# Kernel optimization log

Hardware: AMD Instinct MI355X
Metric: run time of the kernel (lower is better)

The kernel has to match this reference:

```python
import jax, jax.numpy as jnp
import numpy as np
from jax import lax

H = 8          # num_heads
STATE = 16     # SSM state_dim
EPS = 1e-5


def layer_norm(x, g, b):
    mu = jnp.mean(x, axis=-1, keepdims=True)
    var = jnp.mean((x - mu) ** 2, axis=-1, keepdims=True)
    return (x - mu) / jnp.sqrt(var + EPS) * g + b


def linear(x, w, b):
    # torch nn.Linear convention: w [out,in]
    return x @ w.T + b


def cross_attn(q_in, kv_in, qw, qb, kw, kb, vw, vb, ow, ob, g, beta):
    B, Lq, D = q_in.shape
    Lk = kv_in.shape[1]
    hd = D // H
    Q = linear(q_in, qw, qb).reshape(B, Lq, H, hd).transpose(0, 2, 1, 3)
    K = linear(kv_in, kw, kb).reshape(B, Lk, H, hd).transpose(0, 2, 1, 3)
    V = linear(kv_in, vw, vb).reshape(B, Lk, H, hd).transpose(0, 2, 1, 3)
    scores = jnp.einsum('bhqd,bhkd->bhqk', Q, K) / (hd ** 0.5)
    w = jax.nn.softmax(scores, axis=-1)
    out = jnp.einsum('bhqk,bhkd->bhqd', w, V)
    out = out.transpose(0, 2, 1, 3).reshape(B, Lq, D)
    out = linear(out, ow, ob)
    out = layer_norm(out + q_in, g, beta)
    return out, w


def ssm(x, in_w, in_b, A, Bm, C, gw, gb, ow, ob):
    B, L, D = x.shape
    xp = linear(x, in_w, in_b)                      # [B,L,2D]
    x_in = xp[..., D:]                              # second chunk
    gate = jax.nn.sigmoid(linear(x, gw, gb))
    x_in = x_in * gate
    def step(h, xt):
        h = h @ A.T + xt @ Bm.T                     # [B,STATE]
        return h, h @ C.T                           # y [B,D]
    h0 = jnp.zeros((B, STATE), dtype=x.dtype)
    _, ys = lax.scan(step, h0, x_in.transpose(1, 0, 2))
    ys = ys.transpose(1, 0, 2)
    return linear(ys, ow, ob)


def mamba_block(x, p, i):
    y = ssm(layer_norm(x, p['m_ln1_g'][i], p['m_ln1_b'][i]),
            p['m_in_w'][i], p['m_in_b'][i], p['m_A'][i], p['m_B'][i], p['m_C'][i],
            p['m_gate_w'][i], p['m_gate_b'][i], p['m_sout_w'][i], p['m_sout_b'][i])
    x = x + y
    h = layer_norm(x, p['m_ln2_g'][i], p['m_ln2_b'][i])
    h = linear(h, p['m_f1_w'][i], p['m_f1_b'][i])
    h = jax.nn.gelu(h, approximate=False)
    h = linear(h, p['m_f2_w'][i], p['m_f2_b'][i])
    return x + h


def setup_inputs() -> dict:
    key = jax.random.key(0)
    ks = iter(jax.random.split(key, 64))
    B, L, D, BD, VD = 1024, 32, 256, 128, 256
    nB = 6
    def rn(shape, s=0.02):
        return jax.random.normal(next(ks), shape, dtype=jnp.float32) * s
    inp = {
        'ble_features': jax.random.normal(next(ks), (B, L, BD), dtype=jnp.float32),
        'visual_features': jax.random.normal(next(ks), (B, L, VD), dtype=jnp.float32),
        # modality projections
        'bp_w': rn((D, BD)), 'bp_b': jnp.zeros(D), 'bp_emb': rn((D,)),
        'bp_g': jnp.ones(D), 'bp_beta': jnp.zeros(D),
        'vp_w': rn((D, VD)), 'vp_b': jnp.zeros(D), 'vp_emb': rn((D,)),
        'vp_g': jnp.ones(D), 'vp_beta': jnp.zeros(D),
        # two cross-attentions stacked on axis 0: [0]=ble->vis, [1]=vis->ble
        'a_qw': rn((2, D, D)), 'a_qb': jnp.zeros((2, D)),
        'a_kw': rn((2, D, D)), 'a_kb': jnp.zeros((2, D)),
        'a_vw': rn((2, D, D)), 'a_vb': jnp.zeros((2, D)),
        'a_ow': rn((2, D, D)), 'a_ob': jnp.zeros((2, D)),
        'a_g': jnp.ones((2, D)), 'a_beta': jnp.zeros((2, D)),
        # 6 mamba blocks stacked on axis 0
        'm_ln1_g': jnp.ones((nB, D)), 'm_ln1_b': jnp.zeros((nB, D)),
        'm_in_w': rn((nB, 2 * D, D)), 'm_in_b': jnp.zeros((nB, 2 * D)),
        'm_A': rn((nB, STATE, STATE)), 'm_B': rn((nB, STATE, D)), 'm_C': rn((nB, D, STATE)),
        'm_gate_w': rn((nB, D, D)), 'm_gate_b': jnp.zeros((nB, D)),
        'm_sout_w': rn((nB, D, D)), 'm_sout_b': jnp.zeros((nB, D)),
        'm_ln2_g': jnp.ones((nB, D)), 'm_ln2_b': jnp.zeros((nB, D)),
        'm_f1_w': rn((nB, 4 * D, D)), 'm_f1_b': jnp.zeros((nB, 4 * D)),
        'm_f2_w': rn((nB, D, 4 * D)), 'm_f2_b': jnp.zeros((nB, D)),
        # final projection
        'fin_g': jnp.ones(D), 'fin_beta': jnp.zeros(D),
        'fin_w': rn((D, D)), 'fin_b': jnp.zeros(D),
    }
    return inp


def reference(ble_features, visual_features,
              bp_w, bp_b, bp_emb, bp_g, bp_beta,
              vp_w, vp_b, vp_emb, vp_g, vp_beta,
              a_qw, a_qb, a_kw, a_kb, a_vw, a_vb, a_ow, a_ob, a_g, a_beta,
              m_ln1_g, m_ln1_b, m_in_w, m_in_b, m_A, m_B, m_C,
              m_gate_w, m_gate_b, m_sout_w, m_sout_b,
              m_ln2_g, m_ln2_b, m_f1_w, m_f1_b, m_f2_w, m_f2_b,
              fin_g, fin_beta, fin_w, fin_b):
    ble = layer_norm(linear(ble_features, bp_w, bp_b) + bp_emb, bp_g, bp_beta)
    vis = layer_norm(linear(visual_features, vp_w, vp_b) + vp_emb, vp_g, vp_beta)
    # seq_len == target_length -> align_sequences is identity
    ble_att, w_b2v = cross_attn(ble, vis, a_qw[0], a_qb[0], a_kw[0], a_kb[0],
                                a_vw[0], a_vb[0], a_ow[0], a_ob[0], a_g[0], a_beta[0])
    vis_att, w_v2b = cross_attn(vis, ble, a_qw[1], a_qb[1], a_kw[1], a_kb[1],
                                a_vw[1], a_vb[1], a_ow[1], a_ob[1], a_g[1], a_beta[1])
    fused = ble_att + vis_att
    p = dict(m_ln1_g=m_ln1_g, m_ln1_b=m_ln1_b, m_in_w=m_in_w, m_in_b=m_in_b,
             m_A=m_A, m_B=m_B, m_C=m_C, m_gate_w=m_gate_w, m_gate_b=m_gate_b,
             m_sout_w=m_sout_w, m_sout_b=m_sout_b, m_ln2_g=m_ln2_g, m_ln2_b=m_ln2_b,
             m_f1_w=m_f1_w, m_f1_b=m_f1_b, m_f2_w=m_f2_w, m_f2_b=m_f2_b)
    for i in range(m_A.shape[0]):
        fused = mamba_block(fused, p, i)
    g = jnp.mean(fused, axis=1)
    g = layer_norm(g, fin_g, fin_beta)
    g = jax.nn.gelu(linear(g, fin_w, fin_b), approximate=False)
    wb = jnp.mean(w_b2v, axis=(1, 2, 3))
    wv = jnp.mean(w_v2b, axis=(1, 2, 3))
    tot = wb + wv + 1e-6
    return (g, wb / tot, wv / tot)
```

## Files before the change

### kernel.cpp

```cpp
#include <hip/hip_runtime.h>
#include <hip/hip_bf16.h>
#include <math.h>

static constexpr int Bsz  = 1024;
static constexpr int Lseq = 32;
static constexpr int Dm   = 256;
static constexpr int NROW = Bsz * Lseq;

typedef __attribute__((ext_vector_type(8))) short bf16x8;
typedef __attribute__((ext_vector_type(4))) float f32x4;

__device__ __forceinline__ float sigm_f(float x) {
    return 1.0f / (1.0f + __expf(-x));
}
__device__ __forceinline__ float gelu_f(float x) {
    const float u = x * (0.7978845608028654f + 0.0356774081f * x * x);
    return x * sigm_f(2.0f * u);
}
__device__ __forceinline__ float b2f(ushort u) {
    union { float f; uint v; } t; t.v = ((uint)u) << 16; return t.f;
}
__device__ __forceinline__ ushort f2b(float f) {
    union { float f; uint v; } t; t.f = f;
    const uint lsb = (t.v >> 16) & 1u;
    t.v += 0x7fffu + lsb;
    return (ushort)(t.v >> 16);
}

#define GLDS(gp, lp) __builtin_amdgcn_global_load_lds( \
    (const __attribute__((address_space(1))) void*)(gp), \
    (__attribute__((address_space(3))) void*)(lp), 16, 0, 0)

template<int ACT, bool OUTBF, int OMAP, int DUAL>
__global__ __launch_bounds__(256)
void mgemm(const ushort* __restrict__ X, const ushort* __restrict__ W,
           const ushort* __restrict__ W2,
           const float* __restrict__ b1, const float* __restrict__ b2,
           float* __restrict__ Cf, ushort* __restrict__ Cb,
           ushort* __restrict__ Cb2, int K, int M)
{
    __shared__ ushort As[128 * 32];
    __shared__ ushort Bs[128 * 32];
    __shared__ ushort Bs2[DUAL ? 128 * 32 : 8];
    const int tid = threadIdx.x;
    const int w = tid >> 6, l = tid & 63;
    const int n0 = blockIdx.y << 7;
    const int m0 = blockIdx.x << 7;

    const int ric  = l >> 2;
    const int slot = l & 3;
    const int rL0 = (w << 4) + ric;
    const int rL1 = rL0 + 64;
    const int sw0 = slot ^ ((rL0 >> 1) & 3);
    const int sw1 = slot ^ ((rL1 >> 1) & 3);
    const ushort* gA0 = X + (size_t)(n0 + rL0) * K + (sw0 << 3);
    const ushort* gA1 = X + (size_t)(n0 + rL1) * K + (sw1 << 3);
    const ushort* gB0 = W + (size_t)(m0 + rL0) * K + (sw0 << 3);
    const ushort* gB1 = W + (size_t)(m0 + rL1) * K + (sw1 << 3);
    const ushort* gC0 = nullptr; const ushort* gC1 = nullptr;
    if constexpr (DUAL) {
        gC0 = W2 + (size_t)(m0 + rL0) * K + (sw0 << 3);
        gC1 = W2 + (size_t)(m0 + rL1) * K + (sw1 << 3);
    }
    ushort* lA0 = As + ((size_t)w << 9);
    ushort* lA1 = As + ((size_t)(w + 4) << 9);
    ushort* lB0 = Bs + ((size_t)w << 9);
    ushort* lB1 = Bs + ((size_t)(w + 4) << 9);
    ushort* lC0 = Bs2 + ((size_t)w << 9);
    ushort* lC1 = Bs2 + ((size_t)(w + 4) << 9);

    const int wr = (w >> 1) & 1, wc = w & 1;
    const int cl = l & 15, kg = l >> 4;
    int aoff[4], boff[4];
    #pragma unroll
    for (int m = 0; m < 4; ++m) {
        const int r = wr * 64 + m * 16 + cl;
        aoff[m] = r * 32 + ((kg ^ ((r >> 1) & 3)) << 3);
    }
    #pragma unroll
    for (int n = 0; n < 4; ++n) {
        const int r = wc * 64 + n * 16 + cl;
        boff[n] = r * 32 + ((kg ^ ((r >> 1) & 3)) << 3);
    }

    f32x4 acc[4][4];
    f32x4 acc2[DUAL ? 4 : 1][DUAL ? 4 : 1];
    #pragma unroll
    for (int m = 0; m < 4; ++m)
        #pragma unroll
        for (int n = 0; n < 4; ++n) {
            acc[m][n] = (f32x4){0.f, 0.f, 0.f, 0.f};
            if constexpr (DUAL) acc2[m][n] = (f32x4){0.f, 0.f, 0.f, 0.f};
        }

    for (int kc = 0; kc < K; kc += 32) {
        GLDS(gA0, lA0); GLDS(gA1, lA1);
        GLDS(gB0, lB0); GLDS(gB1, lB1);
        gA0 += 32; gA1 += 32; gB0 += 32; gB1 += 32;
        if constexpr (DUAL) {
            GLDS(gC0, lC0); GLDS(gC1, lC1);
            gC0 += 32; gC1 += 32;
        }
        __syncthreads();
        bf16x8 av[4], bv[4];
        #pragma unroll
        for (int m = 0; m < 4; ++m) av[m] = *(const bf16x8*)(As + aoff[m]);
        #pragma unroll
        for (int n = 0; n < 4; ++n) bv[n] = *(const bf16x8*)(Bs + boff[n]);
        #pragma unroll
        for (int m = 0; m < 4; ++m)
            #pragma unroll
            for (int n = 0; n < 4; ++n)
                acc[m][n] = __builtin_amdgcn_mfma_f32_16x16x32_bf16(
                    av[m], bv[n], acc[m][n], 0, 0, 0);
        if constexpr (DUAL) {
            bf16x8 cv[4];
            #pragma unroll
            for (int n = 0; n < 4; ++n) cv[n] = *(const bf16x8*)(Bs2 + boff[n]);
            #pragma unroll
            for (int m = 0; m < 4; ++m)
                #pragma unroll
                for (int n = 0; n < 4; ++n)
                    acc2[m][n] = __builtin_amdgcn_mfma_f32_16x16x32_bf16(
                        av[m], cv[n], acc2[m][n], 0, 0, 0);
        }
        __syncthreads();
    }

    const int colb = m0 + wc * 64 + cl;
    const int rowb = n0 + wr * 64 + (kg << 2);
    float biasA[4], biasB[4];
    #pragma unroll
    for (int n = 0; n < 4; ++n) {
        biasA[n] = (b1 != nullptr) ? b1[colb + n * 16] : 0.0f;
        if constexpr (DUAL) biasB[n] = b2[colb + n * 16];
    }
    #pragma unroll
    for (int m = 0; m < 4; ++m) {
        #pragma unroll
        for (int j = 0; j < 4; ++j) {
            const size_t row = (size_t)(rowb + m * 16 + j);
            #pragma unroll
            for (int n = 0; n < 4; ++n) {
                const int col = colb + n * 16;
                size_t idx;
                if (OMAP == 1) idx = row * 1024 + ((size_t)(col >> 4) << 5) + (col & 15);
                else           idx = row * (size_t)M + col;
                const float vA = acc[m][n][j] + biasA[n];
                if constexpr (DUAL == 1) {
                    const float vB = acc2[m][n][j] + biasB[n];
                    Cb[idx] = f2b(sigm_f(vA) * vB);
                } else if constexpr (DUAL == 2) {
                    Cb[idx]  = f2b(vA);
                    Cb2[idx] = f2b(acc2[m][n][j] + biasB[n]);
                } else {
                    float v = vA;
                    if (ACT == 1) v = sigm_f(v);
                    else if (ACT == 2) v = gelu_f(v);
                    if (OUTBF) Cb[idx] = f2b(v);
                    else       Cf[idx] = v;
                }
            }
        }
    }
}

template<bool ADD_E, bool ACC_F, bool WRV, int LNOUT, bool HASB2>
__global__ __launch_bounds__(256)
void growln_k(const ushort* __restrict__ X, const ushort* __restrict__ W,
              const float* __restrict__ b1, const float* __restrict__ b2,
              const float* __restrict__ E, const float* __restrict__ g,
              const float* __restrict__ bt, float* __restrict__ Fres,
              ushort* __restrict__ Yb, int K)
{
    __shared__ ushort As[64 * 32];
    __shared__ ushort Bs[256 * 32];
    const int tid = threadIdx.x;
    const int w = tid >> 6, l = tid & 63;
    const int n0 = blockIdx.x << 6;

    const int ric = l >> 2, slot = l & 3;
    const int rA  = (w << 4) + ric;
    const int swA = slot ^ ((rA >> 1) & 3);
    const ushort* gA = X + (size_t)(n0 + rA) * K + (swA << 3);
    ushort* lA = As + (w << 9);
    const int rB0 = (w << 4) + ric;
    const int rB1 = rB0 + 64, rB2 = rB0 + 128, rB3 = rB0 + 192;
    const ushort* gB0 = W + (size_t)rB0 * K + ((slot ^ ((rB0 >> 1) & 3)) << 3);
    const ushort* gB1 = W + (size_t)rB1 * K + ((slot ^ ((rB1 >> 1) & 3)) << 3);
    const ushort* gB2 = W + (size_t)rB2 * K + ((slot ^ ((rB2 >> 1) & 3)) << 3);
    const ushort* gB3 = W + (size_t)rB3 * K + ((slot ^ ((rB3 >> 1) & 3)) << 3);
    ushort* lB0 = Bs + (w << 9);
    ushort* lB1 = Bs + ((4 + w) << 9);
    ushort* lB2 = Bs + ((8 + w) << 9);
    ushort* lB3 = Bs + ((12 + w) << 9);

    const int cl = l & 15, kg = l >> 4;
    const int ar = (w << 4) + cl;
    const int aoff = ar * 32 + ((kg ^ ((ar >> 1) & 3)) << 3);
    int boff[16];
    #pragma unroll
    for (int n = 0; n < 16; ++n) {
        const int br = n * 16 + cl;
        boff[n] = br * 32 + ((kg ^ ((br >> 1) & 3)) << 3);
    }

    f32x4 acc[16];
    #pragma unroll
    for (int n = 0; n < 16; ++n) acc[n] = (f32x4){0.f, 0.f, 0.f, 0.f};

    for (int kc = 0; kc < K; kc += 32) {
        GLDS(gA, lA);   gA  += 32;
        GLDS(gB0, lB0); gB0 += 32;
        GLDS(gB1, lB1); gB1 += 32;
        GLDS(gB2, lB2); gB2 += 32;
        GLDS(gB3, lB3); gB3 += 32;
        __syncthreads();
        const bf16x8 av = *(const bf16x8*)(As + aoff);
        #pragma unroll
        for (int n = 0; n < 16; ++n) {
            const bf16x8 bv = *(const bf16x8*)(Bs + boff[n]);
            acc[n] = __builtin_amdgcn_mfma_f32_16x16x32_bf16(av, bv, acc[n], 0, 0, 0);
        }
        __syncthreads();
    }

    float bA[16];
    #pragma unroll
    for (int n = 0; n < 16; ++n) {
        float v = (b1 != nullptr) ? b1[n * 16 + cl] : 0.0f;
        if (HASB2) v += b2[n * 16 + cl];
        bA[n] = v;
    }
    float gg[16], bb[16];
    if (LNOUT > 0) {
        #pragma unroll
        for (int n = 0; n < 16; ++n) { gg[n] = g[n * 16 + cl]; bb[n] = bt[n * 16 + cl]; }
    }

    #pragma unroll
    for (int j = 0; j < 4; ++j) {
        const int r = n0 + (w << 4) + (kg << 2) + j;
        const size_t rb = (size_t)r << 8;
        float v[16];
        float s = 0.0f;
        #pragma unroll
        for (int n = 0; n < 16; ++n) {
            float x = acc[n][j] + bA[n];
            if (ADD_E) x += E[rb + n * 16 + cl];
            if (ACC_F) x += Fres[rb + n * 16 + cl];
            v[n] = x; s += x;
        }
        if (WRV) {
            #pragma unroll
            for (int n = 0; n < 16; ++n) Fres[rb + n * 16 + cl] = v[n];
        }
        if (LNOUT > 0) {
            #pragma unroll
            for (int o = 1; o < 16; o <<= 1) s += __shfl_xor(s, o);
            const float mu = s * (1.0f / 256.0f);
            float q = 0.0f;
            #pragma unroll
            for (int n = 0; n < 16; ++n) { const float d = v[n] - mu; q += d * d; }
            #pragma unroll
            for (int o = 1; o < 16; o <<= 1) q += __shfl_xor(q, o);
            const float rstd = rsqrtf(q * (1.0f / 256.0f) + 1e-5f);
            #pragma unroll
            for (int n = 0; n < 16; ++n) {
                const float y = (v[n] - mu) * rstd * gg[n] + bb[n];
                const size_t idx = rb + n * 16 + cl;
                if (LNOUT & 1) Yb[idx] = f2b(y);
                if (LNOUT == 2 || LNOUT == 3) Fres[idx] = y;
                if (LNOUT == 4) Fres[idx] += y;
            }
        }
    }
}

__global__ __launch_bounds__(256)
void ln_k(const float* __restrict__ X, const float* __restrict__ g,
          const float* __restrict__ bt, ushort* __restrict__ Yb)
{
    const int lane = threadIdx.x & 63;
    const int row  = (blockIdx.x << 2) + (threadIdx.x >> 6);
    const size_t base = (size_t)row * Dm + (lane << 2);
    float4 v = *reinterpret_cast<const float4*>(&X[base]);
    float s = v.x + v.y + v.z + v.w;
    #pragma unroll
    for (int o = 1; o < 64; o <<= 1) s += __shfl_xor(s, o);
    const float mu = s * (1.0f / 256.0f);
    const float d0 = v.x - mu, d1 = v.y - mu, d2 = v.z - mu, d3 = v.w - mu;
    float q = d0*d0 + d1*d1 + d2*d2 + d3*d3;
    #pragma unroll
    for (int o = 1; o < 64; o <<= 1) q += __shfl_xor(q, o);
    const float rstd = rsqrtf(q * (1.0f / 256.0f) + 1e-5f);
    const int c = lane << 2;
    const float4 gg = *reinterpret_cast<const float4*>(&g[c]);
    const float4 bb = *reinterpret_cast<const float4*>(&bt[c]);
    ushort4 ub;
    ub.x = f2b(d0*rstd*gg.x + bb.x); ub.y = f2b(d1*rstd*gg.y + bb.y);
    ub.z = f2b(d2*rstd*gg.z + bb.z); ub.w = f2b(d3*rstd*gg.w + bb.w);
    *reinterpret_cast<ushort4*>(&Yb[base]) = ub;
}

__global__ __launch_bounds__(256)
void attn_k(const ushort* __restrict__ Q, const ushort* __restrict__ K,
            const ushort* __restrict__ V, ushort* __restrict__ O)
{
    __shared__ float Qs[32][33], Ks[32][33], Vs[32][33], Ss[32][33];
    const int bh = blockIdx.x;
    const int b = bh >> 3, h = bh & 7;
    const int tid = threadIdx.x;
    const int r  = tid >> 3;
    const int c4 = (tid & 7) << 2;
    const size_t base = ((size_t)b * Lseq + r) * Dm + h * 32 + c4;
    {
        const ushort4 q = *reinterpret_cast<const ushort4*>(&Q[base]);
        Qs[r][c4+0]=b2f(q.x); Qs[r][c4+1]=b2f(q.y); Qs[r][c4+2]=b2f(q.z); Qs[r][c4+3]=b2f(q.w);
        const ushort4 k = *reinterpret_cast<const ushort4*>(&K[base]);
        Ks[r][c4+0]=b2f(k.x); Ks[r][c4+1]=b2f(k.y); Ks[r][c4+2]=b2f(k.z); Ks[r][c4+3]=b2f(k.w);
        const ushort4 v = *reinterpret_cast<const ushort4*>(&V[base]);
        Vs[r][c4+0]=b2f(v.x); Vs[r][c4+1]=b2f(v.y); Vs[r][c4+2]=b2f(v.z); Vs[r][c4+3]=b2f(v.w);
    }
    __syncthreads();
    float sc[4] = {0.f, 0.f, 0.f, 0.f};
    #pragma unroll
    for (int d = 0; d < 32; ++d) {
        const float qv = Qs[r][d];
        #pragma unroll
        for (int j = 0; j < 4; ++j) sc[j] = fmaf(qv, Ks[c4+j][d], sc[j]);
    }
    #pragma unroll
    for (int j = 0; j < 4; ++j) sc[j] *= 0.17677669529663687f;
    float mx = fmaxf(fmaxf(sc[0], sc[1]), fmaxf(sc[2], sc[3]));
    #pragma unroll
    for (int o = 1; o < 8; o <<= 1) mx = fmaxf(mx, __shfl_xor(mx, o));
    float sum = 0.f;
    #pragma unroll
    for (int j = 0; j < 4; ++j) { sc[j] = __expf(sc[j] - mx); sum += sc[j]; }
    #pragma unroll
    for (int o = 1; o < 8; o <<= 1) sum += __shfl_xor(sum, o);
    const float inv = 1.0f / sum;
    #pragma unroll
    for (int j = 0; j < 4; ++j) Ss[r][c4+j] = sc[j] * inv;
    __syncthreads();
    float o4[4] = {0.f, 0.f, 0.f, 0.f};
    #pragma unroll
    for (int k = 0; k < 32; ++k) {
        const float wv = Ss[r][k];
        #pragma unroll
        for (int j = 0; j < 4; ++j) o4[j] = fmaf(wv, Vs[k][c4+j], o4[j]);
    }
    ushort4 ob; ob.x=f2b(o4[0]); ob.y=f2b(o4[1]); ob.z=f2b(o4[2]); ob.w=f2b(o4[3]);
    *reinterpret_cast<ushort4*>(&O[base]) = ob;
}

__global__ __launch_bounds__(256)
void xb_gemm(const ushort* __restrict__ X, const ushort* __restrict__ Bw,
             ushort* __restrict__ XB)
{
    __shared__ ushort As[128 * 32];
    __shared__ ushort Bsf[16 * 256];
    const int tid = threadIdx.x;
    const int w = tid >> 6, l = tid & 63;
    const int n0 = blockIdx.x << 7;
    #pragma unroll
    for (int rep = 0; rep < 2; ++rep) {
        const int u = (rep << 8) + tid;
        const int r = u >> 5;
        const int c8 = (u & 31) << 3;
        const int di = (r * 256 + c8) ^ ((r & 7) << 3);
        *(bf16x8*)(Bsf + di) = *(const bf16x8*)(Bw + r * 256 + c8);
    }
    const int ric = l >> 2, slot = l & 3;
    const int rL0 = (w << 4) + ric, rL1 = rL0 + 64;
    const int sw0 = slot ^ ((rL0 >> 1) & 3), sw1 = slot ^ ((rL1 >> 1) & 3);
    const ushort* gA0 = X + (size_t)(n0 + rL0) * 256 + (sw0 << 3);
    const ushort* gA1 = X + (size_t)(n0 + rL1) * 256 + (sw1 << 3);
    ushort* lA0 = As + (w << 9);
    ushort* lA1 = As + ((w + 4) << 9);
    const int cl = l & 15, kg = l >> 4;
    int aoff[2];
    #pragma unroll
    for (int m = 0; m < 2; ++m) {
        const int r = w * 32 + m * 16 + cl;
        aoff[m] = r * 32 + ((kg ^ ((r >> 1) & 3)) << 3);
    }
    f32x4 acc[2] = {(f32x4){0.f,0.f,0.f,0.f}, (f32x4){0.f,0.f,0.f,0.f}};
    for (int kc = 0; kc < 256; kc += 32) {
        GLDS(gA0, lA0); GLDS(gA1, lA1);
        gA0 += 32; gA1 += 32;
        __syncthreads();
        const bf16x8 av0 = *(const bf16x8*)(As + aoff[0]);
        const bf16x8 av1 = *(const bf16x8*)(As + aoff[1]);
        const int bidx = (cl * 256 + kc + (kg << 3)) ^ ((cl & 7) << 3);
        const bf16x8 bv = *(const bf16x8*)(Bsf + bidx);
        acc[0] = __builtin_amdgcn_mfma_f32_16x16x32_bf16(av0, bv, acc[0], 0, 0, 0);
        acc[1] = __builtin_amdgcn_mfma_f32_16x16x32_bf16(av1, bv, acc[1], 0, 0, 0);
        __syncthreads();
    }
    #pragma unroll
    for (int m = 0; m < 2; ++m)
        #pragma unroll
        for (int j = 0; j < 4; ++j) {
            const int row = n0 + w * 32 + m * 16 + (kg << 2) + j;
            XB[(size_t)row * 16 + cl] = f2b(acc[m][j]);
        }
}

__global__ __launch_bounds__(256)
void powT_k(const float* __restrict__ A_all, ushort* __restrict__ T_all)
{
    __shared__ float P[2][16][16];
    __shared__ float Asm[16][16];
    const int layer = blockIdx.x;
    const float* A = A_all + layer * 256;
    ushort* T = T_all + (size_t)layer * 262144;
    const int tid = threadIdx.x;
    const int i = tid >> 4, j = tid & 15;
    Asm[i][j] = A[tid];
    const bf16x8 z = {0,0,0,0,0,0,0,0};
    for (int u = tid; u < 32768; u += 256)
        *(bf16x8*)(T + (size_t)u * 8) = z;
    P[0][i][j] = (i == j) ? 1.0f : 0.0f;
    __syncthreads();
    for (int k = 0; k < 32; ++k) {
        const float pv = P[k & 1][i][j];
        const ushort pb = f2b(pv);
        for (int tau = 0; tau + k < 32; ++tau)
            T[(size_t)((tau + k) * 16 + i) * 512 + tau * 16 + j] = pb;
        float acc = 0.0f;
        #pragma unroll
        for (int l2 = 0; l2 < 16; ++l2) acc = fmaf(P[k & 1][i][l2], Asm[l2][j], acc);
        P[(k & 1) ^ 1][i][j] = acc;
        __syncthreads();
    }
}

__global__ __launch_bounds__(256)
void zeroH_k(ushort* __restrict__ Hp)
{
    const int i = blockIdx.x * 256 + threadIdx.x;
    const bf16x8 z = {0,0,0,0,0,0,0,0};
    *(bf16x8*)(Hp + (size_t)i * 8) = z;
}

__global__ __launch_bounds__(256)
void wsc_k(const float* __restrict__ sw, const float* __restrict__ Cc,
           ushort* __restrict__ Wp)
{
    const int i = blockIdx.x >> 4;
    const int m = ((blockIdx.x & 15) << 4) + (threadIdx.x >> 4);
    const int s = threadIdx.x & 15;
    const float* swr = sw + ((size_t)i << 16) + (m << 8);
    const float* cc  = Cc + ((size_t)i << 12) + s;
    float acc = 0.0f;
    #pragma unroll 8
    for (int d = 0; d < 256; ++d) acc = fmaf(swr[d], cc[d << 4], acc);
    ushort* o = Wp + ((size_t)i << 13) + (m << 5);
    o[s] = f2b(acc);
    o[s + 16] = 0;
}

__global__ __launch_bounds__(256)
void meanL_k(const float* __restrict__ X, float* __restrict__ G)
{
    const int idx = blockIdx.x * 256 + threadIdx.x;
    const int b = idx >> 8, d = idx & 255;
    const float* xp = X + (size_t)b * (Lseq * Dm) + d;
    float s = 0.0f;
    #pragma unroll
    for (int t = 0; t < Lseq; ++t) s += xp[t << 8];
    G[idx] = s * (1.0f / 32.0f);
}

__global__ __launch_bounds__(256)
void fillw_k(float* __restrict__ out)
{
    const int i = blockIdx.x * 256 + threadIdx.x;
    const float wm = 1.0f / 32.0f;
    out[i] = wm / (wm + wm + 1e-6f);
}

__global__ __launch_bounds__(256)
void cast_k(const float* __restrict__ src, ushort* __restrict__ dst, int n4)
{
    const int i = blockIdx.x * 256 + threadIdx.x;
    if (i < n4) {
        const float4 v = reinterpret_cast<const float4*>(src)[i];
        ushort4 o; o.x = f2b(v.x); o.y = f2b(v.y); o.z = f2b(v.z); o.w = f2b(v.w);
        reinterpret_cast<ushort4*>(dst)[i] = o;
    }
}

__global__ __launch_bounds__(256)
void cast_inw_k(const float* __restrict__ src, ushort* __restrict__ dst)
{
    const int i = blockIdx.x * 256 + threadIdx.x;
    const int blk = i >> 14, rem = i & 16383;
    const float4 v = reinterpret_cast<const float4*>(
        src + (size_t)blk * 131072 + 65536)[rem];
    ushort4 o; o.x = f2b(v.x); o.y = f2b(v.y); o.z = f2b(v.z); o.w = f2b(v.w);
    reinterpret_cast<ushort4*>(dst)[i] = o;
}

extern "C" void kernel_launch(void* const* d_in, const int* in_sizes, int n_in,
                              void* d_out, int out_size, void* d_ws, size_t ws_size,
                              hipStream_t stream)
{
    const float* ble_f   = (const float*)d_in[0];
    const float* vis_f   = (const float*)d_in[1];
    const float* bp_w    = (const float*)d_in[2];
    const float* bp_b    = (const float*)d_in[3];
    const float* bp_emb  = (const float*)d_in[4];
    const float* bp_g    = (const float*)d_in[5];
    const float* bp_beta = (const float*)d_in[6];
    const float* vp_w    = (const float*)d_in[7];
    const float* vp_b    = (const float*)d_in[8];
    const float* vp_emb  = (const float*)d_in[9];
    const float* vp_g    = (const float*)d_in[10];
    const float* vp_beta = (const float*)d_in[11];
    const float* a_qw    = (const float*)d_in[12];
    const float* a_qb    = (const float*)d_in[13];
    const float* a_kw    = (const float*)d_in[14];
    const float* a_kb    = (const float*)d_in[15];
    const float* a_vw    = (const float*)d_in[16];
    const float* a_vb    = (const float*)d_in[17];
    const float* a_ow    = (const float*)d_in[18];
    const float* a_ob    = (const float*)d_in[19];
    const float* a_g     = (const float*)d_in[20];
    const float* a_beta  = (const float*)d_in[21];
    const float* m_ln1_g = (const float*)d_in[22];
    const float* m_ln1_b = (const float*)d_in[23];
    const float* m_in_w  = (const float*)d_in[24];
    const float* m_in_b  = (const float*)d_in[25];
    const float* m_A     = (const float*)d_in[26];
    const float* m_B     = (const float*)d_in[27];
    const float* m_C     = (const float*)d_in[28];
    const float* m_gw    = (const float*)d_in[29];
    const float* m_gb    = (const float*)d_in[30];
    const float* m_sw    = (const float*)d_in[31];
    const float* m_sb    = (const float*)d_in[32];
    const float* m_ln2_g = (const float*)d_in[33];
    const float* m_ln2_b = (const float*)d_in[34];
    const float* m_f1w   = (const float*)d_in[35];
    const float* m_f1b   = (const float*)d_in[36];
    const float* m_f2w   = (const float*)d_in[37];
    const float* m_f2b   = (const float*)d_in[38];
    const float* fin_g   = (const float*)d_in[39];
    const float* fin_beta= (const float*)d_in[40];
    const float* fin_w   = (const float*)d_in[41];
    const float* fin_b   = (const float*)d_in[42];

    float* out = (float*)d_out;
    float* ws  = (float*)d_ws;
    const size_t NDf = (size_t)NROW * Dm;

    float* F_res = ws;
    float* F0 = ws + 1 * NDf;
    float* F1 = ws + 2 * NDf;
    float* F2 = ws + 3 * NDf;
    ushort* S0 = (ushort*)(ws + 4 * NDf);
    ushort* S1 = S0 + NDf;
    ushort* S2 = S1 + NDf;
    ushort* S3 = S2 + NDf;
    ushort* S4 = S3 + NDf;
    ushort* Wa = S4 + NDf;
    ushort* W_bp  = Wa;
    ushort* W_vp  = W_bp + 32768;
    ushort* W_q   = W_vp + 65536;
    ushort* W_k   = W_q + 131072;
    ushort* W_v   = W_k + 131072;
    ushort* W_o   = W_v + 131072;
    ushort* W_g   = W_o + 131072;
    ushort* W_in  = W_g + 393216;
    ushort* W_f1  = W_in + 393216;
    ushort* W_f2  = W_f1 + 1572864;
    ushort* W_fin = W_f2 + 1572864;
    ushort* W_sc  = W_fin + 65536;
    ushort* Hpad  = W_sc + 49152;
    ushort* B_ble = (ushort*)F2;
    ushort* B_vis = B_ble + (size_t)NROW * 128;
    ushort* T_all = (ushort*)F2;
    ushort* W_bm  = T_all + 1572864;
    ushort* XBuf  = W_bm + 24576;

    const dim3 blk(256);
    auto cgrid = [](int n4) { return dim3((n4 + 255) / 256); };

    cast_k<<<cgrid(1048576), blk, 0, stream>>>(ble_f, B_ble, 1048576);
    cast_k<<<cgrid(2097152), blk, 0, stream>>>(vis_f, B_vis, 2097152);
    cast_k<<<cgrid(8192),   blk, 0, stream>>>(bp_w, W_bp, 8192);
    cast_k<<<cgrid(16384),  blk, 0, stream>>>(vp_w, W_vp, 16384);
    cast_k<<<cgrid(32768),  blk, 0, stream>>>(a_qw, W_q, 32768);
    cast_k<<<cgrid(32768),  blk, 0, stream>>>(a_kw, W_k, 32768);
    cast_k<<<cgrid(32768),  blk, 0, stream>>>(a_vw, W_v, 32768);
    cast_k<<<cgrid(32768),  blk, 0, stream>>>(a_ow, W_o, 32768);
    cast_k<<<cgrid(98304),  blk, 0, stream>>>(m_gw, W_g, 98304);
    cast_k<<<cgrid(393216), blk, 0, stream>>>(m_f1w, W_f1, 393216);
    cast_k<<<cgrid(393216), blk, 0, stream>>>(m_f2w, W_f2, 393216);
    cast_k<<<cgrid(16384),  blk, 0, stream>>>(fin_w, W_fin, 16384);
    cast_inw_k<<<cgrid(98304), blk, 0, stream>>>(m_in_w, W_in);
    wsc_k<<<96, blk, 0, stream>>>(m_sw, m_C, W_sc);

    auto gg = [](int M, int N) { return dim3(M / 128, N / 128); };
    const dim3 gRow(NROW / 64);

    growln_k<false,false,false,3,true><<<gRow, blk, 0, stream>>>(
        B_ble, W_bp, bp_b, bp_emb, nullptr, bp_g, bp_beta, F0, S0, 128);
    growln_k<false,false,false,3,true><<<gRow, blk, 0, stream>>>(
        B_vis, W_vp, vp_b, vp_emb, nullptr, vp_g, vp_beta, F1, S1, 256);

    for (int a = 0; a < 2; ++a) {
        const ushort* qin_b = (a == 0) ? S0 : S1;
        const ushort* kin_b = (a == 0) ? S1 : S0;
        const float*  qin_f = (a == 0) ? F0 : F1;
        const size_t wo = (size_t)a * 65536;
        const size_t bo = (size_t)a * 256;
        mgemm<0,true,0,0><<<gg(256, NROW), blk, 0, stream>>>(
            qin_b, W_q + wo, nullptr, a_qb + bo, nullptr, nullptr, S4, nullptr, 256, 256);
        mgemm<0,true,0,2><<<gg(256, NROW), blk, 0, stream>>>(
            kin_b, W_k + wo, W_v + wo, a_kb + bo, a_vb + bo, nullptr, S2, S3, 256, 256);
        attn_k<<<Bsz * 8, blk, 0, stream>>>(S4, S2, S3, S4);
        if (a == 0)
            growln_k<true,false,false,2,false><<<gRow, blk, 0, stream>>>(
                S4, W_o + wo, a_ob + bo, nullptr, qin_f, a_g + bo, a_beta + bo, F_res, nullptr, 256);
        else
            growln_k<true,false,false,4,false><<<gRow, blk, 0, stream>>>(
                S4, W_o + wo, a_ob + bo, nullptr, qin_f, a_g + bo, a_beta + bo, F_res, nullptr, 256);
    }

    powT_k<<<6, blk, 0, stream>>>(m_A, T_all);
    cast_k<<<cgrid(6144), blk, 0, stream>>>(m_B, W_bm, 6144);
    zeroH_k<<<512, blk, 0, stream>>>(Hpad);

    ln_k<<<NROW/4, blk, 0, stream>>>(F_res, m_ln1_g, m_ln1_b, S0);

    for (int i = 0; i < 6; ++i) {
        mgemm<0,true,0,1><<<gg(256, NROW), blk, 0, stream>>>(
            S0, W_g + (size_t)i*65536, W_in + (size_t)i*65536,
            m_gb + i*256, m_in_b + (size_t)i*512 + 256, nullptr, S2, nullptr, 256, 256);
        xb_gemm<<<NROW/128, blk, 0, stream>>>(S2, W_bm + (size_t)i*4096, XBuf);
        mgemm<0,true,1,0><<<gg(512, 1024), blk, 0, stream>>>(
            XBuf, T_all + (size_t)i*262144, nullptr, nullptr, nullptr, nullptr, Hpad, nullptr, 512, 512);
        growln_k<false,true,true,1,false><<<gRow, blk, 0, stream>>>(
            Hpad, W_sc + (size_t)i*8192, m_sb + i*256, nullptr, nullptr,
            m_ln2_g + i*256, m_ln2_b + i*256, F_res, S0, 32);
        mgemm<2,true,0,0><<<gg(1024, NROW), blk, 0, stream>>>(
            S0, W_f1 + (size_t)i*262144, nullptr, m_f1b + i*1024, nullptr, nullptr, S1, nullptr, 256, 1024);
        if (i < 5)
            growln_k<false,true,true,1,false><<<gRow, blk, 0, stream>>>(
                S1, W_f2 + (size_t)i*262144, m_f2b + i*256, nullptr, nullptr,
                m_ln1_g + (i+1)*256, m_ln1_b + (i+1)*256, F_res, S0, 1024);
        else
            growln_k<false,true,true,0,false><<<gRow, blk, 0, stream>>>(
                S1, W_f2 + (size_t)i*262144, m_f2b + i*256, nullptr, nullptr,
                nullptr, nullptr, F_res, nullptr, 1024);
    }

    meanL_k<<<(Bsz * Dm) / 256, blk, 0, stream>>>(F_res, F0);
    ln_k<<<Bsz/4, blk, 0, stream>>>(F0, fin_g, fin_beta, S1);
    mgemm<2,false,0,0><<<gg(256, Bsz), blk, 0, stream>>>(
        S1, W_fin, nullptr, fin_b, nullptr, out, nullptr, nullptr, 256, 256);
    fillw_k<<<8, blk, 0, stream>>>(out + (size_t)Bsz * Dm);
}
```

Baseline: 1.321 ms.

## Fuse SSM output projection, LN2, FFN up/down and LN1 into one kernel

Replaces three per-layer launches (SSM output GEMM with residual and LN2, the FFN1 GEMM with GELU, and the FFN2 GEMM with residual and next LN1) with a single row-block kernel. Each 64-row block keeps the normalized activations and a 128-wide hidden chunk in LDS and accumulates the down-projection in registers, so the 1024-wide hidden tensor never goes to global memory. The cost is that every block re-streams the full W1 and W2 weights, and the loads are not double-buffered. Large register and LDS use may also reduce occupancy. growln_k loses the template options that are now unused.

```diff
diff --git a/kernel.cpp b/kernel.cpp
--- a/kernel.cpp
+++ b/kernel.cpp
@@ -165,7 +165,7 @@
     }
 }
 
-template<bool ADD_E, bool ACC_F, bool WRV, int LNOUT, bool HASB2>
+template<bool ADD_E, int LNOUT, bool HASB2>
 __global__ __launch_bounds__(256)
 void growln_k(const ushort* __restrict__ X, const ushort* __restrict__ W,
               const float* __restrict__ b1, const float* __restrict__ b2,
@@ -233,10 +233,8 @@
         bA[n] = v;
     }
     float gg[16], bb[16];
-    if (LNOUT > 0) {
-        #pragma unroll
-        for (int n = 0; n < 16; ++n) { gg[n] = g[n * 16 + cl]; bb[n] = bt[n * 16 + cl]; }
-    }
+    #pragma unroll
+    for (int n = 0; n < 16; ++n) { gg[n] = g[n * 16 + cl]; bb[n] = bt[n * 16 + cl]; }
 
     #pragma unroll
     for (int j = 0; j < 4; ++j) {
@@ -248,30 +246,194 @@
         for (int n = 0; n < 16; ++n) {
             float x = acc[n][j] + bA[n];
             if (ADD_E) x += E[rb + n * 16 + cl];
-            if (ACC_F) x += Fres[rb + n * 16 + cl];
             v[n] = x; s += x;
         }
-        if (WRV) {
-            #pragma unroll
-            for (int n = 0; n < 16; ++n) Fres[rb + n * 16 + cl] = v[n];
-        }
-        if (LNOUT > 0) {
+        #pragma unroll
+        for (int o = 1; o < 16; o <<= 1) s += __shfl_xor(s, o);
+        const float mu = s * (1.0f / 256.0f);
+        float q = 0.0f;
+        #pragma unroll
+        for (int n = 0; n < 16; ++n) { const float d = v[n] - mu; q += d * d; }
+        #pragma unroll
+        for (int o = 1; o < 16; o <<= 1) q += __shfl_xor(q, o);
+        const float rstd = rsqrtf(q * (1.0f / 256.0f) + 1e-5f);
+        #pragma unroll
+        for (int n = 0; n < 16; ++n) {
+            const float y = (v[n] - mu) * rstd * gg[n] + bb[n];
+            const size_t idx = rb + n * 16 + cl;
+            if (LNOUT == 3) Yb[idx] = f2b(y);
+            if (LNOUT == 2 || LNOUT == 3) Fres[idx] = y;
+            if (LNOUT == 4) Fres[idx] += y;
+        }
+    }
+}
+
+template<bool LN1>
+__global__ __launch_bounds__(256)
+void ffn_k(const ushort* __restrict__ Hp, const ushort* __restrict__ Wsc,
+           const float* __restrict__ sb,
+           const float* __restrict__ ln2g, const float* __restrict__ ln2b,
+           const ushort* __restrict__ W1, const float* __restrict__ f1bias,
+           const ushort* __restrict__ W2, const float* __restrict__ f2bias,
+           const float* __restrict__ ln1g, const float* __restrict__ ln1b,
+           float* __restrict__ Fres, ushort* __restrict__ S0out)
+{
+    __shared__ ushort xnS[64 * 256];
+    __shared__ ushort hidS[64 * 128];
+    __shared__ ushort stA[64 * 32];
+    __shared__ ushort stB[256 * 32];
+    const int tid = threadIdx.x;
+    const int w = tid >> 6, l = tid & 63;
+    const int n0 = blockIdx.x << 6;
+    const int cl = l & 15, kg = l >> 4;
+    const int ric = l >> 2, slot = l & 3;
+
+    {
+        const int rA = (w << 4) + ric;
+        GLDS(Hp + (size_t)(n0 + rA) * 32 + ((slot ^ ((rA >> 1) & 3)) << 3), stA + (w << 9));
+        #pragma unroll
+        for (int c = 0; c < 4; ++c) {
+            const int rB = ((w + 4 * c) << 4) + ric;
+            GLDS(Wsc + (size_t)rB * 32 + ((slot ^ ((rB >> 1) & 3)) << 3), stB + ((w + 4 * c) << 9));
+        }
+    }
+    f32x4 acc[16];
+    #pragma unroll
+    for (int n = 0; n < 16; ++n) acc[n] = (f32x4){0.f, 0.f, 0.f, 0.f};
+    int boff[16];
+    #pragma unroll
+    for (int n = 0; n < 16; ++n) {
+        const int br = n * 16 + cl;
+        boff[n] = br * 32 + ((kg ^ ((br >> 1) & 3)) << 3);
+    }
+    __syncthreads();
+    {
+        const int ar = (w << 4) + cl;
+        const bf16x8 av = *(const bf16x8*)(stA + ar * 32 + ((kg ^ ((ar >> 1) & 3)) << 3));
+        #pragma unroll
+        for (int n = 0; n < 16; ++n) {
+            const bf16x8 bv = *(const bf16x8*)(stB + boff[n]);
+            acc[n] = __builtin_amdgcn_mfma_f32_16x16x32_bf16(av, bv, acc[n], 0, 0, 0);
+        }
+    }
+    {
+        float sbv[16], g2[16], b2v[16];
+        #pragma unroll
+        for (int n = 0; n < 16; ++n) {
+            sbv[n] = sb[n * 16 + cl];
+            g2[n] = ln2g[n * 16 + cl]; b2v[n] = ln2b[n * 16 + cl];
+        }
+        #pragma unroll
+        for (int j = 0; j < 4; ++j) {
+            const int lr = (w << 4) + (kg << 2) + j;
+            const size_t rb = (size_t)(n0 + lr) << 8;
+            float s = 0.0f;
+            #pragma unroll
+            for (int n = 0; n < 16; ++n) {
+                acc[n][j] += sbv[n] + Fres[rb + n * 16 + cl];
+                s += acc[n][j];
+            }
             #pragma unroll
             for (int o = 1; o < 16; o <<= 1) s += __shfl_xor(s, o);
             const float mu = s * (1.0f / 256.0f);
             float q = 0.0f;
             #pragma unroll
-            for (int n = 0; n < 16; ++n) { const float d = v[n] - mu; q += d * d; }
+            for (int n = 0; n < 16; ++n) { const float d = acc[n][j] - mu; q += d * d; }
             #pragma unroll
             for (int o = 1; o < 16; o <<= 1) q += __shfl_xor(q, o);
             const float rstd = rsqrtf(q * (1.0f / 256.0f) + 1e-5f);
             #pragma unroll
             for (int n = 0; n < 16; ++n) {
-                const float y = (v[n] - mu) * rstd * gg[n] + bb[n];
-                const size_t idx = rb + n * 16 + cl;
-                if (LNOUT & 1) Yb[idx] = f2b(y);
-                if (LNOUT == 2 || LNOUT == 3) Fres[idx] = y;
-                if (LNOUT == 4) Fres[idx] += y;
+                const float y = (acc[n][j] - mu) * rstd * g2[n] + b2v[n];
+                const int col = n * 16 + cl;
+                xnS[lr * 256 + (((col >> 3) ^ (lr & 7)) << 3) + (col & 7)] = f2b(y);
+            }
+        }
+    }
+    __syncthreads();
+
+    const int xr = (w << 4) + cl;
+    for (int c = 0; c < 8; ++c) {
+        f32x4 hacc[8];
+        #pragma unroll
+        for (int n = 0; n < 8; ++n) hacc[n] = (f32x4){0.f, 0.f, 0.f, 0.f};
+        for (int kc = 0; kc < 256; kc += 32) {
+            const int rB0 = (w << 4) + ric, rB1 = rB0 + 64;
+            GLDS(W1 + (size_t)(c * 128 + rB0) * 256 + kc + ((slot ^ ((rB0 >> 1) & 3)) << 3), stB + (w << 9));
+            GLDS(W1 + (size_t)(c * 128 + rB1) * 256 + kc + ((slot ^ ((rB1 >> 1) & 3)) << 3), stB + ((w + 4) << 9));
+            __syncthreads();
+            const int c8b = (kc >> 3) + kg;
+            const bf16x8 av = *(const bf16x8*)(xnS + xr * 256 + ((c8b ^ (xr & 7)) << 3));
+            #pragma unroll
+            for (int n = 0; n < 8; ++n) {
+                const bf16x8 bv = *(const bf16x8*)(stB + boff[n]);
+                hacc[n] = __builtin_amdgcn_mfma_f32_16x16x32_bf16(av, bv, hacc[n], 0, 0, 0);
+            }
+            __syncthreads();
+        }
+        #pragma unroll
+        for (int n = 0; n < 8; ++n) {
+            const float hb = f1bias[c * 128 + n * 16 + cl];
+            #pragma unroll
+            for (int j = 0; j < 4; ++j) {
+                const int lr = (w << 4) + (kg << 2) + j;
+                const int col = n * 16 + cl;
+                hidS[lr * 128 + (((col >> 3) ^ (lr & 7)) << 3) + (col & 7)] =
+                    f2b(gelu_f(hacc[n][j] + hb));
+            }
+        }
+        __syncthreads();
+        for (int kc2 = 0; kc2 < 128; kc2 += 32) {
+            #pragma unroll
+            for (int cc = 0; cc < 4; ++cc) {
+                const int rB = ((w + 4 * cc) << 4) + ric;
+                GLDS(W2 + (size_t)rB * 1024 + c * 128 + kc2 + ((slot ^ ((rB >> 1) & 3)) << 3),
+                     stB + ((w + 4 * cc) << 9));
+            }
+            __syncthreads();
+            const int h8 = (kc2 >> 3) + kg;
+            const bf16x8 av = *(const bf16x8*)(hidS + xr * 128 + ((h8 ^ (xr & 7)) << 3));
+            #pragma unroll
+            for (int n = 0; n < 16; ++n) {
+                const bf16x8 bv = *(const bf16x8*)(stB + boff[n]);
+                acc[n] = __builtin_amdgcn_mfma_f32_16x16x32_bf16(av, bv, acc[n], 0, 0, 0);
+            }
+            __syncthreads();
+        }
+    }
+
+    {
+        float fb[16], g1[16], b1v[16];
+        #pragma unroll
+        for (int n = 0; n < 16; ++n) {
+            fb[n] = f2bias[n * 16 + cl];
+            if (LN1) { g1[n] = ln1g[n * 16 + cl]; b1v[n] = ln1b[n * 16 + cl]; }
+        }
+        #pragma unroll
+        for (int j = 0; j < 4; ++j) {
+            const int lr = (w << 4) + (kg << 2) + j;
+            const size_t rb = (size_t)(n0 + lr) << 8;
+            float v[16];
+            float s = 0.0f;
+            #pragma unroll
+            for (int n = 0; n < 16; ++n) {
+                v[n] = acc[n][j] + fb[n];
+                Fres[rb + n * 16 + cl] = v[n];
+                s += v[n];
+            }
+            if (LN1) {
+                #pragma unroll
+                for (int o = 1; o < 16; o <<= 1) s += __shfl_xor(s, o);
+                const float mu = s * (1.0f / 256.0f);
+                float q = 0.0f;
+                #pragma unroll
+                for (int n = 0; n < 16; ++n) { const float d = v[n] - mu; q += d * d; }
+                #pragma unroll
+                for (int o = 1; o < 16; o <<= 1) q += __shfl_xor(q, o);
+                const float rstd = rsqrtf(q * (1.0f / 256.0f) + 1e-5f);
+                #pragma unroll
+                for (int n = 0; n < 16; ++n)
+                    S0out[rb + n * 16 + cl] = f2b((v[n] - mu) * rstd * g1[n] + b1v[n]);
             }
         }
     }
@@ -606,9 +768,9 @@
     auto gg = [](int M, int N) { return dim3(M / 128, N / 128); };
     const dim3 gRow(NROW / 64);
 
-    growln_k<false,false,false,3,true><<<gRow, blk, 0, stream>>>(
+    growln_k<false,3,true><<<gRow, blk, 0, stream>>>(
         B_ble, W_bp, bp_b, bp_emb, nullptr, bp_g, bp_beta, F0, S0, 128);
-    growln_k<false,false,false,3,true><<<gRow, blk, 0, stream>>>(
+    growln_k<false,3,true><<<gRow, blk, 0, stream>>>(
         B_vis, W_vp, vp_b, vp_emb, nullptr, vp_g, vp_beta, F1, S1, 256);
 
     for (int a = 0; a < 2; ++a) {
@@ -623,10 +785,10 @@
             kin_b, W_k + wo, W_v + wo, a_kb + bo, a_vb + bo, nullptr, S2, S3, 256, 256);
         attn_k<<<Bsz * 8, blk, 0, stream>>>(S4, S2, S3, S4);
         if (a == 0)
-            growln_k<true,false,false,2,false><<<gRow, blk, 0, stream>>>(
+            growln_k<true,2,false><<<gRow, blk, 0, stream>>>(
                 S4, W_o + wo, a_ob + bo, nullptr, qin_f, a_g + bo, a_beta + bo, F_res, nullptr, 256);
         else
-            growln_k<true,false,false,4,false><<<gRow, blk, 0, stream>>>(
+            growln_k<true,4,false><<<gRow, blk, 0, stream>>>(
                 S4, W_o + wo, a_ob + bo, nullptr, qin_f, a_g + bo, a_beta + bo, F_res, nullptr, 256);
     }
 
@@ -643,19 +805,20 @@
         xb_gemm<<<NROW/128, blk, 0, stream>>>(S2, W_bm + (size_t)i*4096, XBuf);
         mgemm<0,true,1,0><<<gg(512, 1024), blk, 0, stream>>>(
             XBuf, T_all + (size_t)i*262144, nullptr, nullptr, nullptr, nullptr, Hpad, nullptr, 512, 512);
-        growln_k<false,true,true,1,false><<<gRow, blk, 0, stream>>>(
-            Hpad, W_sc + (size_t)i*8192, m_sb + i*256, nullptr, nullptr,
-            m_ln2_g + i*256, m_ln2_b + i*256, F_res, S0, 32);
-        mgemm<2,true,0,0><<<gg(1024, NROW), blk, 0, stream>>>(
-            S0, W_f1 + (size_t)i*262144, nullptr, m_f1b + i*1024, nullptr, nullptr, S1, nullptr, 256, 1024);
         if (i < 5)
-            growln_k<false,true,true,1,false><<<gRow, blk, 0, stream>>>(
-                S1, W_f2 + (size_t)i*262144, m_f2b + i*256, nullptr, nullptr,
-                m_ln1_g + (i+1)*256, m_ln1_b + (i+1)*256, F_res, S0, 1024);
+            ffn_k<true><<<gRow, blk, 0, stream>>>(
+                Hpad, W_sc + (size_t)i*8192, m_sb + i*256,
+                m_ln2_g + i*256, m_ln2_b + i*256,
+                W_f1 + (size_t)i*262144, m_f1b + i*1024,
+                W_f2 + (size_t)i*262144, m_f2b + i*256,
+                m_ln1_g + (i+1)*256, m_ln1_b + (i+1)*256, F_res, S0);
         else
-            growln_k<false,true,true,0,false><<<gRow, blk, 0, stream>>>(
-                S1, W_f2 + (size_t)i*262144, m_f2b + i*256, nullptr, nullptr,
-                nullptr, nullptr, F_res, nullptr, 1024);
+            ffn_k<false><<<gRow, blk, 0, stream>>>(
+                Hpad, W_sc + (size_t)i*8192, m_sb + i*256,
+                m_ln2_g + i*256, m_ln2_b + i*256,
+                W_f1 + (size_t)i*262144, m_f1b + i*1024,
+                W_f2 + (size_t)i*262144, m_f2b + i*256,
+                nullptr, nullptr, F_res, nullptr);
     }
 
     meanL_k<<<(Bsz * Dm) / 256, blk, 0, stream>>>(F_res, F0);
```

Result: slower. 1.766 ms (+33.7%).

## Stage GEMM bf16 epilogue through LDS for vectorized stores and remap workgroups

Applied to the files above, without the earlier changes.

The bf16-output and dual-weight GEMM epilogue now writes each warp's 64x64 result tile into swizzled shared memory, then reads it back as 8-element vectors and issues 16-byte global stores instead of scattered 2-byte stores. Workgroup IDs are also remapped in groups of 8, to change which tiles run together and improve cache locality. The cost is extra LDS traffic and a larger shared-memory footprint (an additional Rx buffer), which may lower occupancy.

```diff
diff --git a/kernel.cpp b/kernel.cpp
--- a/kernel.cpp
+++ b/kernel.cpp
@@ -39,13 +39,18 @@
            float* __restrict__ Cf, ushort* __restrict__ Cb,
            ushort* __restrict__ Cb2, int K, int M)
 {
-    __shared__ ushort As[128 * 32];
-    __shared__ ushort Bs[128 * 32];
-    __shared__ ushort Bs2[DUAL ? 128 * 32 : 8];
+    __shared__ ushort As[4096];
+    __shared__ ushort Bs[4096];
+    __shared__ ushort Bs2[DUAL ? 4096 : 8];
+    __shared__ ushort Rx[DUAL ? 4096 : 8192];
     const int tid = threadIdx.x;
     const int w = tid >> 6, l = tid & 63;
-    const int n0 = blockIdx.y << 7;
-    const int m0 = blockIdx.x << 7;
+
+    int f = blockIdx.y * gridDim.x + blockIdx.x;
+    const int nwg = gridDim.x * gridDim.y;
+    if ((nwg & 7) == 0) f = (f & 7) * (nwg >> 3) + (f >> 3);
+    const int n0 = (f / gridDim.x) << 7;
+    const int m0 = (f % gridDim.x) << 7;
 
     const int ric  = l >> 2;
     const int slot = l & 3;
@@ -135,33 +140,63 @@
         biasA[n] = (b1 != nullptr) ? b1[colb + n * 16] : 0.0f;
         if constexpr (DUAL) biasB[n] = b2[colb + n * 16];
     }
-    #pragma unroll
-    for (int m = 0; m < 4; ++m) {
-        #pragma unroll
-        for (int j = 0; j < 4; ++j) {
-            const size_t row = (size_t)(rowb + m * 16 + j);
-            #pragma unroll
-            for (int n = 0; n < 4; ++n) {
-                const int col = colb + n * 16;
+
+    if constexpr (OUTBF || DUAL != 0) {
+        ushort* Rw;
+        if constexpr (DUAL) Rw = (w == 0) ? As : (w == 1) ? Bs : (w == 2) ? Bs2 : Rx;
+        else                Rw = (w == 0) ? As : (w == 1) ? Bs : Rx + ((w - 2) << 12);
+        const int rr = l >> 3, rc8 = (l & 7) << 3;
+        const int nout = (DUAL == 2) ? 2 : 1;
+        for (int which = 0; which < nout; ++which) {
+            #pragma unroll
+            for (int m = 0; m < 4; ++m)
+                #pragma unroll
+                for (int j = 0; j < 4; ++j) {
+                    const int lrow = m * 16 + (kg << 2) + j;
+                    #pragma unroll
+                    for (int n = 0; n < 4; ++n) {
+                        float v;
+                        if (which == 0) {
+                            v = acc[m][n][j] + biasA[n];
+                            if constexpr (DUAL == 1)
+                                v = sigm_f(v) * (acc2[m][n][j] + biasB[n]);
+                            else if (ACT == 1) v = sigm_f(v);
+                            else if (ACT == 2) v = gelu_f(v);
+                        } else {
+                            v = acc2[m][n][j] + biasB[n];
+                        }
+                        const int lcol = (n << 4) + cl;
+                        Rw[lrow * 64 + (lcol ^ (((lrow >> 1) & 7) << 3))] = f2b(v);
+                    }
+                }
+            ushort* dst = (which == 0) ? Cb : Cb2;
+            #pragma unroll
+            for (int p = 0; p < 8; ++p) {
+                const int lrow = (p << 3) + rr;
+                const bf16x8 v8 = *(const bf16x8*)(
+                    Rw + lrow * 64 + (rc8 ^ (((lrow >> 1) & 7) << 3)));
+                const size_t grow = (size_t)(n0 + wr * 64 + lrow);
+                const int gcol = m0 + wc * 64 + rc8;
                 size_t idx;
-                if (OMAP == 1) idx = row * 1024 + ((size_t)(col >> 4) << 5) + (col & 15);
-                else           idx = row * (size_t)M + col;
-                const float vA = acc[m][n][j] + biasA[n];
-                if constexpr (DUAL == 1) {
-                    const float vB = acc2[m][n][j] + biasB[n];
-                    Cb[idx] = f2b(sigm_f(vA) * vB);
-                } else if constexpr (DUAL == 2) {
-                    Cb[idx]  = f2b(vA);
-                    Cb2[idx] = f2b(acc2[m][n][j] + biasB[n]);
-                } else {
-                    float v = vA;
+                if (OMAP == 1) idx = grow * 1024 + ((size_t)(gcol >> 4) << 5) + (gcol & 15);
+                else           idx = grow * (size_t)M + gcol;
+                *(bf16x8*)(dst + idx) = v8;
+            }
+        }
+    } else {
+        #pragma unroll
+        for (int m = 0; m < 4; ++m)
+            #pragma unroll
+            for (int j = 0; j < 4; ++j) {
+                const size_t row = (size_t)(rowb + m * 16 + j);
+                #pragma unroll
+                for (int n = 0; n < 4; ++n) {
+                    float v = acc[m][n][j] + biasA[n];
                     if (ACT == 1) v = sigm_f(v);
                     else if (ACT == 2) v = gelu_f(v);
-                    if (OUTBF) Cb[idx] = f2b(v);
-                    else       Cf[idx] = v;
+                    Cf[row * (size_t)M + colb + n * 16] = v;
                 }
             }
-        }
     }
 }
 
```

Measured after the change: 1.306 ms. No clear change (-1.1%).
